# Optimization experiments

Measured on AMD Instinct MI355X. Metric: run time of the kernel, lower is better.

The kernel has to match this reference:

```python
import jax, jax.numpy as jnp
import numpy as np

WIN = 7
K1, K2 = 0.01, 0.03
NP_ = WIN ** 3
COV_NORM = NP_ / (NP_ - 1)


def _box3d(x, win=WIN):
    # Separable box filter: three 1D VALID convs (same math as the dense
    for ax in range(3):
        kshape = [1, 1, 1, 1, 1]
        kshape[2 + ax] = win
        k = jnp.ones(kshape, x.dtype) / win
        x = jax.lax.conv_general_dilated(
            x, k, window_strides=(1, 1, 1), padding='VALID',
            dimension_numbers=('NCDHW', 'OIDHW', 'NCDHW'))
    return x


def setup_inputs() -> dict:
    key = jax.random.key(0)
    k1, k2 = jax.random.split(key)
    B, C, D, H, W = 4, 1, 128, 128, 128
    X = jax.random.normal(k1, (B, C, D, H, W), dtype=jnp.float32)
    Y = jax.random.normal(k2, (B, C, D, H, W), dtype=jnp.float32)
    data_range = jnp.ones((B, 1, 1, 1, 1), dtype=jnp.float32)
    return {"X": X, "Y": Y, "data_range": data_range}


def reference(X, Y, data_range):
    C1 = (K1 * data_range) ** 2
    C2 = (K2 * data_range) ** 2
    ux = _box3d(X)
    uy = _box3d(Y)
    uxx = _box3d(X * X)
    uyy = _box3d(Y * Y)
    uxy = _box3d(X * Y)
    vx = COV_NORM * (uxx - ux * ux)
    vy = COV_NORM * (uyy - uy * uy)
    vxy = COV_NORM * (uxy - ux * uy)
    A1 = 2 * ux * uy + C1
    A2 = 2 * vxy + C2
    B1 = ux ** 2 + uy ** 2 + C1
    B2 = vx + vy + C2
    S = (A1 * A2) / (B1 * B2)
    return S.mean()
```

## Files before the change

kernel.cpp:

```cpp
#include <hip/hip_runtime.h>

#define NFULL 128
#define NOUT  122
#define NBLK  512
#define NTHR  512

#define WROW 34
#define WQ   748
#define WB   3740
#define HROW 34
#define HQ   544
#define HB   2720

__device__ __forceinline__ void phaseA_task(const float* __restrict__ px,
                                            const float* __restrict__ py,
                                            float* __restrict__ wp)
{
    float xs[8], ys[8];
#pragma unroll
    for (int k = 0; k < 4; ++k) {
        float2 tx = *(const float2*)(px + 2 * k);
        float2 ty = *(const float2*)(py + 2 * k);
        xs[2 * k] = tx.x; xs[2 * k + 1] = tx.y;
        ys[2 * k] = ty.x; ys[2 * k + 1] = ty.y;
    }
    float sx = 0.f, sy = 0.f, sxx = 0.f, syy = 0.f, sxy = 0.f;
#pragma unroll
    for (int k = 0; k < 7; ++k) {
        sx += xs[k]; sy += ys[k];
        sxx = fmaf(xs[k], xs[k], sxx);
        syy = fmaf(ys[k], ys[k], syy);
        sxy = fmaf(xs[k], ys[k], sxy);
    }
    float tx2 = sx - xs[0] + xs[7];
    float ty2 = sy - ys[0] + ys[7];
    float txx = sxx - xs[0] * xs[0] + xs[7] * xs[7];
    float tyy = syy - ys[0] * ys[0] + ys[7] * ys[7];
    float txy = sxy - xs[0] * ys[0] + xs[7] * ys[7];
    *(float2*)(wp + 0 * WQ) = make_float2(sx,  tx2);
    *(float2*)(wp + 1 * WQ) = make_float2(sy,  ty2);
    *(float2*)(wp + 2 * WQ) = make_float2(sxx, txx);
    *(float2*)(wp + 3 * WQ) = make_float2(syy, tyy);
    *(float2*)(wp + 4 * WQ) = make_float2(sxy, txy);
}

__global__ __launch_bounds__(NTHR, 4)
void ssim3d_kernel(const float* __restrict__ X, const float* __restrict__ Y,
                   const float* __restrict__ DR, double* __restrict__ ws,
                   float* __restrict__ out, int mode)
{
    __shared__ __align__(16) float wbuf[WB];
    __shared__ __align__(16) float hbuf[HB];
    __shared__ float  redf[8];
    __shared__ double redd[8];
    __shared__ int lastFlag;

    const int tid = threadIdx.x;
    int bi = blockIdx.x;
    const int bb = bi & 3;  bi >>= 2;
    const int ht = bi & 7;  bi >>= 3;
    const int wt = bi & 3;  bi >>= 2;
    const int dc = bi;

    const int h0 = ht << 4;
    const int w0 = (wt == 3) ? 90 : (wt << 5);
    const int w_hi = (wt == 3) ? 122 : ((wt == 2) ? 90 : (w0 + 32));
    const int csize = (dc < 2) ? 31 : 30;
    const int d0 = (dc < 2) ? dc * 31 : 62 + (dc - 2) * 30;
    const int nsl = csize + 6;

    const float dr = DR[bb];
    const float c1s = (0.01f * dr) * (0.01f * dr) * 117649.0f;
    const float c2s = (0.03f * dr) * (0.03f * dr) * 117649.0f;
    const float tni = 1.0f / 343.0f;
    const float kkA = 2.0f * 117649.0f / 342.0f;
    const float kkB = 117649.0f / 342.0f;

    const int aid = tid - 160;
    const int rA  = aid >> 4;
    const int sA  = aid & 15;
    int grA = h0 + rA; if (grA > NFULL - 1) grA = NFULL - 1;
    const int coffA = w0 + 2 * sA;

    const int bq = tid >> 5;
    const int bc = tid & 31;

    const int sC = tid & 31, hC = tid >> 5;
    const int gh = h0 + hC;
    const int gw = w0 + sC;
    const bool vld = (gh < NOUT) && (gw < w_hi);

    const size_t planeStride = (size_t)NFULL * NFULL;
    const size_t bbase = (size_t)bb * NFULL * planeStride;

    float ring[7][5];
    float run[5];
#pragma unroll
    for (int k = 0; k < 7; ++k)
#pragma unroll
        for (int q = 0; q < 5; ++q) ring[k][q] = 0.f;
#pragma unroll
    for (int q = 0; q < 5; ++q) run[q] = 0.f;
    float acc = 0.0f;

    for (int base = 0; base <= nsl; base += 7) {
#pragma unroll
        for (int u = 0; u < 7; ++u) {
            const int s = base + u;
            if (s <= nsl) {
                if (s < nsl && aid >= 0) {
                    const int dIn = d0 + s;
                    const float* Xp = X + bbase + (size_t)dIn * planeStride;
                    const float* Yp = Y + bbase + (size_t)dIn * planeStride;
                    phaseA_task(Xp + grA * NFULL + coffA, Yp + grA * NFULL + coffA,
                                wbuf + rA * WROW + 2 * sA);
                }
                if (s >= 1) {
                    const float* src = hbuf + hC * HROW + sC;
                    const int slot = (u + 6) % 7;
#pragma unroll
                    for (int q = 0; q < 5; ++q) {
                        float v = src[q * HQ];
                        run[q] += v - ring[slot][q];
                        ring[slot][q] = v;
                    }
                    if (s >= 7 && vld) {
                        float Sx  = run[0];
                        float Sy  = run[1];
                        float Sxx = run[2];
                        float Syy = run[3];
                        float Sxy = run[4];
                        float P = Sx * Sy;
                        float Q = fmaf(Sx, Sx, Sy * Sy);
                        float A1 = fmaf(2.f, P, c1s);
                        float A2 = fmaf(kkA, fmaf(-tni, P, Sxy), c2s);
                        float B1 = Q + c1s;
                        float B2 = fmaf(kkB, fmaf(-tni, Q, Sxx + Syy), c2s);
                        float num = A1 * A2;
                        float den = B1 * B2;
                        float r0 = __builtin_amdgcn_rcpf(den);
                        r0 = r0 * fmaf(-den, r0, 2.0f);
                        acc = fmaf(num, r0, acc);
                    }
                }
                __syncthreads();
                if (s < nsl && tid < 160) {
                    const float* srcw = wbuf + bq * WQ + bc;
                    float* dsth = hbuf + bq * HQ + bc;
                    float win = srcw[0] + srcw[WROW] + srcw[2 * WROW]
                              + srcw[3 * WROW] + srcw[4 * WROW] + srcw[5 * WROW];
#pragma unroll
                    for (int h = 0; h < 16; ++h) {
                        win += srcw[(h + 6) * WROW];
                        dsth[h * HROW] = win;
                        win -= srcw[h * WROW];
                    }
                }
                __syncthreads();
            }
        }
    }

#pragma unroll
    for (int off = 32; off; off >>= 1) acc += __shfl_down(acc, off);
    if ((tid & 63) == 0) redf[tid >> 6] = acc;
    __syncthreads();

    if (mode) {
        if (tid == 0) {
            double t = 0.0;
#pragma unroll
            for (int i = 0; i < 8; ++i) t += (double)redf[i];
            ws[blockIdx.x] = t;
            __threadfence();
            unsigned int old = atomicAdd((unsigned int*)(ws + NBLK), 1u);
            lastFlag = (old == NBLK - 1) ? 1 : 0;
        }
        __syncthreads();
        if (lastFlag) {
            __threadfence();
            double t = 0.0;
            for (int i = tid; i < NBLK; i += NTHR) t += ws[i];
#pragma unroll
            for (int off = 32; off; off >>= 1) t += __shfl_down(t, off);
            if ((tid & 63) == 0) redd[tid >> 6] = t;
            __syncthreads();
            if (tid == 0) {
                double r = 0.0;
#pragma unroll
                for (int i = 0; i < 8; ++i) r += redd[i];
                out[0] = (float)(r * (1.0 / 7263392.0));
            }
        }
    } else {
        if (tid == 0) {
            double t = 0.0;
#pragma unroll
            for (int i = 0; i < 8; ++i) t += (double)redf[i];
            atomicAdd(ws, t);
        }
    }
}

__global__ void ssim3d_finalize(const double* __restrict__ ws, float* __restrict__ out)
{
    out[0] = (float)(ws[0] * (1.0 / 7263392.0));
}

extern "C" void kernel_launch(void* const* d_in, const int* in_sizes, int n_in,
                              void* d_out, int out_size, void* d_ws, size_t ws_size,
                              hipStream_t stream)
{
    const float* X  = (const float*)d_in[0];
    const float* Y  = (const float*)d_in[1];
    const float* DR = (const float*)d_in[2];
    double* ws = (double*)d_ws;

    const int mode = (ws_size >= (size_t)(NBLK + 1) * sizeof(double)) ? 1 : 0;
    if (mode)
        hipMemsetAsync((char*)d_ws + (size_t)NBLK * sizeof(double), 0, sizeof(double), stream);
    else
        hipMemsetAsync(d_ws, 0, sizeof(double), stream);

    ssim3d_kernel<<<NBLK, NTHR, 0, stream>>>(X, Y, DR, ws, (float*)d_out, mode);
    if (!mode) ssim3d_finalize<<<1, 1, 0, stream>>>(ws, (float*)d_out);
}
```

Before: 142.2 us.

## Double-buffer stage buffers to pipeline W/H/D passes with one barrier per slice

Double-buffers the W-sum and H-sum shared buffers so the W pass for slice s, the H pass for slice s-1 and the D pass for slice s-2 run in the same step, cutting from two barriers per slice to one. It also issues the global loads before the other stages so their latency overlaps, makes each W-pass thread produce four outputs from ten loaded values, and spreads the H pass over more threads. The depth dimension is split into more chunks (768 blocks, occupancy hint raised to 6) for more parallelism. In exchange it costs more halo reloads in depth, doubles shared memory use, and adds register pressure under the tighter launch bound.

```diff
diff --git a/kernel.cpp b/kernel.cpp
--- a/kernel.cpp
+++ b/kernel.cpp
@@ -2,7 +2,7 @@
 
 #define NFULL 128
 #define NOUT  122
-#define NBLK  512
+#define NBLK  768
 #define NTHR  512
 
 #define WROW 34
@@ -12,45 +12,23 @@
 #define HQ   544
 #define HB   2720
 
-__device__ __forceinline__ void phaseA_task(const float* __restrict__ px,
-                                            const float* __restrict__ py,
-                                            float* __restrict__ wp)
-{
-    float xs[8], ys[8];
-#pragma unroll
-    for (int k = 0; k < 4; ++k) {
-        float2 tx = *(const float2*)(px + 2 * k);
-        float2 ty = *(const float2*)(py + 2 * k);
-        xs[2 * k] = tx.x; xs[2 * k + 1] = tx.y;
-        ys[2 * k] = ty.x; ys[2 * k + 1] = ty.y;
-    }
-    float sx = 0.f, sy = 0.f, sxx = 0.f, syy = 0.f, sxy = 0.f;
-#pragma unroll
-    for (int k = 0; k < 7; ++k) {
-        sx += xs[k]; sy += ys[k];
-        sxx = fmaf(xs[k], xs[k], sxx);
-        syy = fmaf(ys[k], ys[k], syy);
-        sxy = fmaf(xs[k], ys[k], sxy);
-    }
-    float tx2 = sx - xs[0] + xs[7];
-    float ty2 = sy - ys[0] + ys[7];
-    float txx = sxx - xs[0] * xs[0] + xs[7] * xs[7];
-    float tyy = syy - ys[0] * ys[0] + ys[7] * ys[7];
-    float txy = sxy - xs[0] * ys[0] + xs[7] * ys[7];
-    *(float2*)(wp + 0 * WQ) = make_float2(sx,  tx2);
-    *(float2*)(wp + 1 * WQ) = make_float2(sy,  ty2);
-    *(float2*)(wp + 2 * WQ) = make_float2(sxx, txx);
-    *(float2*)(wp + 3 * WQ) = make_float2(syy, tyy);
-    *(float2*)(wp + 4 * WQ) = make_float2(sxy, txy);
-}
-
-__global__ __launch_bounds__(NTHR, 4)
+#define EMIT4(E, OFF) {                                                   \
+    float e0=E(0), e1=E(1), e2=E(2), e3=E(3), e4=E(4);                    \
+    float e5=E(5), e6=E(6), e7=E(7), e8=E(8), e9=E(9);                    \
+    float a = ((e0+e1)+(e2+e3)) + ((e4+e5)+e6);                           \
+    float b = a + e7 - e0;                                                \
+    float c = b + e8 - e1;                                                \
+    float d = c + e9 - e2;                                                \
+    *(float2*)(wp + (OFF))     = make_float2(a, b);                       \
+    *(float2*)(wp + (OFF) + 2) = make_float2(c, d); }
+
+__global__ __launch_bounds__(NTHR, 6)
 void ssim3d_kernel(const float* __restrict__ X, const float* __restrict__ Y,
                    const float* __restrict__ DR, double* __restrict__ ws,
                    float* __restrict__ out, int mode)
 {
-    __shared__ __align__(16) float wbuf[WB];
-    __shared__ __align__(16) float hbuf[HB];
+    __shared__ __align__(16) float wbuf[2 * WB];
+    __shared__ __align__(16) float hbuf[2 * HB];
     __shared__ float  redf[8];
     __shared__ double redd[8];
     __shared__ int lastFlag;
@@ -65,8 +43,8 @@
     const int h0 = ht << 4;
     const int w0 = (wt == 3) ? 90 : (wt << 5);
     const int w_hi = (wt == 3) ? 122 : ((wt == 2) ? 90 : (w0 + 32));
-    const int csize = (dc < 2) ? 31 : 30;
-    const int d0 = (dc < 2) ? dc * 31 : 62 + (dc - 2) * 30;
+    const int csize = (dc < 2) ? 21 : 20;
+    const int d0 = (dc < 2) ? dc * 21 : 42 + (dc - 2) * 20;
     const int nsl = csize + 6;
 
     const float dr = DR[bb];
@@ -76,14 +54,15 @@
     const float kkA = 2.0f * 117649.0f / 342.0f;
     const float kkB = 117649.0f / 342.0f;
 
-    const int aid = tid - 160;
-    const int rA  = aid >> 4;
-    const int sA  = aid & 15;
+    const int rA  = tid >> 3;
+    const int qdA = tid & 7;
     int grA = h0 + rA; if (grA > NFULL - 1) grA = NFULL - 1;
-    const int coffA = w0 + 2 * sA;
-
-    const int bq = tid >> 5;
-    const int bc = tid & 31;
+    const int coffA = w0 + 4 * qdA;
+
+    const int bid = tid - 192;
+    const int bcB = bid & 31;
+    const int bhB = (bid >> 5) & 1;
+    const int bqB = bid >> 6;
 
     const int sC = tid & 31, hC = tid >> 5;
     const int gh = h0 + hC;
@@ -103,28 +82,36 @@
     for (int q = 0; q < 5; ++q) run[q] = 0.f;
     float acc = 0.0f;
 
-    for (int base = 0; base <= nsl; base += 7) {
+    for (int base = 0; base <= nsl + 1; base += 7) {
 #pragma unroll
         for (int u = 0; u < 7; ++u) {
             const int s = base + u;
-            if (s <= nsl) {
-                if (s < nsl && aid >= 0) {
-                    const int dIn = d0 + s;
-                    const float* Xp = X + bbase + (size_t)dIn * planeStride;
-                    const float* Yp = Y + bbase + (size_t)dIn * planeStride;
-                    phaseA_task(Xp + grA * NFULL + coffA, Yp + grA * NFULL + coffA,
-                                wbuf + rA * WROW + 2 * sA);
-                }
-                if (s >= 1) {
-                    const float* src = hbuf + hC * HROW + sC;
-                    const int slot = (u + 6) % 7;
+            if (s <= nsl + 1) {
+                float xs[10], ys[10];
+                const bool doA = (s < nsl) && (tid < 176);
+                if (doA) {
+                    const float* Xp = X + bbase + (size_t)(d0 + s) * planeStride
+                                        + (size_t)grA * NFULL + coffA;
+                    const float* Yp = Y + bbase + (size_t)(d0 + s) * planeStride
+                                        + (size_t)grA * NFULL + coffA;
+#pragma unroll
+                    for (int k = 0; k < 5; ++k) {
+                        float2 tx = *(const float2*)(Xp + 2 * k);
+                        float2 ty = *(const float2*)(Yp + 2 * k);
+                        xs[2 * k] = tx.x; xs[2 * k + 1] = tx.y;
+                        ys[2 * k] = ty.x; ys[2 * k + 1] = ty.y;
+                    }
+                }
+                if (s >= 2) {
+                    const float* src = hbuf + (size_t)((s & 1) * HB) + hC * HROW + sC;
+                    const int slot = (u + 5) % 7;
 #pragma unroll
                     for (int q = 0; q < 5; ++q) {
                         float v = src[q * HQ];
                         run[q] += v - ring[slot][q];
                         ring[slot][q] = v;
                     }
-                    if (s >= 7 && vld) {
+                    if (s >= 8 && vld) {
                         float Sx  = run[0];
                         float Sy  = run[1];
                         float Sxx = run[2];
@@ -143,18 +130,38 @@
                         acc = fmaf(num, r0, acc);
                     }
                 }
-                __syncthreads();
-                if (s < nsl && tid < 160) {
-                    const float* srcw = wbuf + bq * WQ + bc;
-                    float* dsth = hbuf + bq * HQ + bc;
+                if (s >= 1 && s <= nsl && tid >= 192) {
+                    const int p = (s - 1) & 1;
+                    const float* srcw = wbuf + (size_t)(p * WB) + bqB * WQ
+                                      + (bhB * 8) * WROW + bcB;
+                    float* dsth = hbuf + (size_t)(p * HB) + bqB * HQ
+                                      + (bhB * 8) * HROW + bcB;
                     float win = srcw[0] + srcw[WROW] + srcw[2 * WROW]
                               + srcw[3 * WROW] + srcw[4 * WROW] + srcw[5 * WROW];
 #pragma unroll
-                    for (int h = 0; h < 16; ++h) {
-                        win += srcw[(h + 6) * WROW];
-                        dsth[h * HROW] = win;
-                        win -= srcw[h * WROW];
-                    }
+                    for (int j = 0; j < 8; ++j) {
+                        win += srcw[(j + 6) * WROW];
+                        dsth[j * HROW] = win;
+                        win -= srcw[j * WROW];
+                    }
+                }
+                if (doA) {
+                    float* wp = wbuf + (size_t)((s & 1) * WB) + rA * WROW + 4 * qdA;
+#define EX(i)  xs[i]
+#define EY(i)  ys[i]
+#define EXX(i) (xs[i] * xs[i])
+#define EYY(i) (ys[i] * ys[i])
+#define EXY(i) (xs[i] * ys[i])
+                    EMIT4(EX,  0 * WQ)
+                    EMIT4(EY,  1 * WQ)
+                    EMIT4(EXX, 2 * WQ)
+                    EMIT4(EYY, 3 * WQ)
+                    EMIT4(EXY, 4 * WQ)
+#undef EX
+#undef EY
+#undef EXX
+#undef EYY
+#undef EXY
                 }
                 __syncthreads();
             }
```

New measurement: 165.9 us. 16.7% more time.
